# Kernel optimization log

Measured on AMD Instinct MI355X. Metric: run time of the kernel, lower is better.

## Reference

```python
import jax, jax.numpy as jnp
import numpy as np

B, N, L = 1, 2048, 256
H, E = 24, 128
D = H * E          # query_dim = inner_dim = 3072
P = 1536           # added_kv_proj_dim
EPS = 1e-5


def _rope_tables(n, e):
    pos = np.arange(n, dtype=np.float32)
    inv_freq = 1.0 / (10000.0 ** (np.arange(0, e, 2, dtype=np.float32) / e))
    ang = pos[:, None] * inv_freq[None, :]          # [n, e/2]
    ang = np.repeat(ang, 2, axis=-1)                # interleaved pairs -> [n, e]
    return np.cos(ang).astype(np.float32), np.sin(ang).astype(np.float32)


def _trans_mat(e):
    # rotate-pairs matrix: (x @ tm)[2i] = -x[2i+1], (x @ tm)[2i+1] = x[2i]
    tm = np.zeros((e, e), dtype=np.float32)
    idx = np.arange(0, e, 2)
    tm[idx + 1, idx] = -1.0
    tm[idx, idx + 1] = 1.0
    return tm


def setup_inputs() -> dict:
    key = jax.random.key(0)
    ks = jax.random.split(key, 16)
    s = 0.02
    cos, sin = _rope_tables(N, E)
    return {
        "spatial": jax.random.normal(ks[0], (B, N, D), jnp.float32),
        "prompt": jax.random.normal(ks[1], (B, L, P), jnp.float32),
        "w_qkv": jax.random.normal(ks[2], (D, 3 * D), jnp.float32) * s,
        "w_add_qkv": jax.random.normal(ks[3], (P, 3 * D), jnp.float32) * s,
        "b_add_qkv": jax.random.normal(ks[4], (3 * D,), jnp.float32) * s,
        "norm_q_w": jnp.ones((E,), jnp.float32),
        "norm_k_w": jnp.ones((E,), jnp.float32),
        "norm_add_q_w": jnp.ones((E,), jnp.float32),
        "norm_add_k_w": jnp.ones((E,), jnp.float32),
        "w_out": jax.random.normal(ks[5], (D, D), jnp.float32) * s,
        "b_out": jax.random.normal(ks[6], (D,), jnp.float32) * s,
        "w_add_out": jax.random.normal(ks[7], (D, D), jnp.float32) * s,
        "b_add_out": jax.random.normal(ks[8], (D,), jnp.float32) * s,
        "rope_cos": jnp.asarray(cos),
        "rope_sin": jnp.asarray(sin),
        "trans_mat": jnp.asarray(_trans_mat(E)),
        "N": N,
    }


def _rms(x, w):
    return x * jax.lax.rsqrt(jnp.mean(x * x, axis=-1, keepdims=True) + EPS) * w


def _split_heads(x, h, e):
    b, s, _ = x.shape
    return x.reshape(b, s, h, e).transpose(0, 2, 1, 3)  # [B,H,S,E]


def reference(spatial, prompt, w_qkv, w_add_qkv, b_add_qkv,
              norm_q_w, norm_k_w, norm_add_q_w, norm_add_k_w,
              w_out, b_out, w_add_out, b_add_out,
              rope_cos, rope_sin, trans_mat, N):
    e = norm_q_w.shape[0]
    h = w_qkv.shape[1] // (3 * e)
    b, n, _ = spatial.shape

    # fused QKV for spatial stream (no bias)
    q, k, v = jnp.split(spatial @ w_qkv, 3, axis=-1)
    q, k, v = (_split_heads(t, h, e) for t in (q, k, v))   # [B,H,N,E]
    q = _rms(q, norm_q_w)
    k = _rms(k, norm_k_w)

    # fused QKV for prompt stream (with bias)
    aq, ak, av = jnp.split(prompt @ w_add_qkv + b_add_qkv, 3, axis=-1)
    aq, ak, av = (_split_heads(t, h, e) for t in (aq, ak, av))  # [B,H,L,E]
    aq = _rms(aq, norm_add_q_w)
    ak = _rms(ak, norm_add_k_w)

    # RoPE on spatial q/k: x*cos + (x@trans_mat)*sin
    def rope(x):
        return x * rope_cos + jnp.einsum('bhne,ef->bhnf', x, trans_mat) * rope_sin
    q = rope(q)
    k = rope(k)

    # joint attention, 'rear' strategy: prompt KV appended after spatial KV
    qf = jnp.concatenate([q, aq], axis=2)   # [B,H,N+L,E]
    kf = jnp.concatenate([k, ak], axis=2)
    vf = jnp.concatenate([v, av], axis=2)
    scale = 1.0 / jnp.sqrt(jnp.float32(e))
    scores = jnp.einsum('bhqe,bhke->bhqk', qf, kf) * scale
    attn = jax.nn.softmax(scores, axis=-1)
    out = jnp.einsum('bhqk,bhke->bhqe', attn, vf)           # [B,H,N+L,E]

    def merge(x):
        return x.transpose(0, 2, 1, 3).reshape(b, x.shape[2], h * e)

    spatial_out = merge(out[:, :, :n]) @ w_out + b_out      # [B,N,D]
    prompt_out = merge(out[:, :, n:]) @ w_add_out + b_add_out  # [B,L,D]
    return spatial_out, prompt_out
```

## Files before the change

kernel.cpp:

```cpp
#include <hip/hip_runtime.h>
#include <cstdint>
#include <cstddef>

typedef __attribute__((ext_vector_type(8))) short short8;
typedef __attribute__((ext_vector_type(4))) float f32x4;
typedef __attribute__((ext_vector_type(16))) float f32x16;

#define DEVI static __device__ __forceinline__

DEVI float bf2f(unsigned short b) {
  union { unsigned int u; float f; } v; v.u = ((unsigned int)b) << 16; return v.f;
}
DEVI unsigned short f2bf(float f) {
  union { float f; unsigned int u; } v; v.f = f;
  unsigned int r = v.u + 0x7fffu + ((v.u >> 16) & 1u);
  return (unsigned short)(r >> 16);
}
DEVI unsigned int pk2(float a, float b) {
  union { float f; unsigned int u; } ua, ub; ua.f = a; ub.f = b;
  return ((ua.u + 0x8000u) >> 16) | ((ub.u + 0x8000u) & 0xffff0000u);
}

DEVI void gload16(const void* g, void* l) {
  __builtin_amdgcn_global_load_lds(
      (const __attribute__((address_space(1))) void*)g,
      (__attribute__((address_space(3))) void*)l, 16, 0, 0);
}

DEVI void drain_ldsdma() {
  asm volatile("s_waitcnt vmcnt(0)" ::: "memory");
  __builtin_amdgcn_sched_barrier(0);
}

DEVI void tr_body(const float* in, unsigned short* out, int Kd, int Nd,
                  int n0, int k0, unsigned short (*tile)[72], int t)
{
  int r = t >> 2, cg = (t & 3) * 16;
  const float* src = in + (size_t)(k0 + r) * Nd + n0 + cg;
#pragma unroll
  for (int q = 0; q < 16; q += 4) {
    float4 f = *(const float4*)(src + q);
    ushort4 u;
    u.x = f2bf(f.x); u.y = f2bf(f.y); u.z = f2bf(f.z); u.w = f2bf(f.w);
    *(ushort4*)&tile[r][cg + q] = u;
  }
  __syncthreads();
  unsigned int p[8];
#pragma unroll
  for (int q = 0; q < 8; ++q)
    p[q] = (unsigned int)tile[cg + 2*q][r] | ((unsigned int)tile[cg + 2*q + 1][r] << 16);
  unsigned short* dst = out + (size_t)(n0 + r) * Kd + k0 + cg;
  *(uint4*)dst       = make_uint4(p[0], p[1], p[2], p[3]);
  *(uint4*)(dst + 8) = make_uint4(p[4], p[5], p[6], p[7]);
}

__global__ __launch_bounds__(256) void prep(
    const float* __restrict__ spatial, unsigned short* __restrict__ spat_bf,
    const float* __restrict__ prompt,  unsigned short* __restrict__ prom_bf,
    const float* __restrict__ w_qkv,   const float* __restrict__ w_add_qkv,
    unsigned short* __restrict__ wTq,  unsigned short* __restrict__ wTaq)
{
  __shared__ unsigned short tile[64][72];
  const int b = blockIdx.x;
  if (b < 2048) {
    const int n4a = 2048 * 3072 / 4, n4b = 256 * 1536 / 4;
    int i = b * 256 + threadIdx.x;
    int stride = 2048 * 256;
    int total = n4a + n4b;
    for (; i < total; i += stride) {
      const float4* src = (i < n4a) ? &((const float4*)spatial)[i]
                                    : &((const float4*)prompt)[i - n4a];
      ushort4* dst = (i < n4a) ? &((ushort4*)spat_bf)[i] : &((ushort4*)prom_bf)[i - n4a];
      float4 f = *src;
      ushort4 u;
      u.x = f2bf(f.x); u.y = f2bf(f.y); u.z = f2bf(f.z); u.w = f2bf(f.w);
      *dst = u;
    }
  } else {
    int bb = b - 2048;
    int bx = bb % 144, y = bb / 144;
    const float* in;  unsigned short* out;  int Kd, k0;
    if (y < 48) { in = w_qkv;     out = wTq;  Kd = 3072; k0 = y * 64; }
    else        { in = w_add_qkv; out = wTaq; Kd = 1536; k0 = (y - 48) * 64; }
    tr_body(in, out, Kd, 9216, bx * 64, k0, tile, threadIdx.x);
  }
}

__global__ __launch_bounds__(256) void transpose_wout(
    const float* __restrict__ w_out, const float* __restrict__ w_add_out,
    unsigned short* __restrict__ wTo, unsigned short* __restrict__ wTao)
{
  __shared__ unsigned short tile[64][72];
  const float* in = blockIdx.z ? w_add_out : w_out;
  unsigned short* out = blockIdx.z ? wTao : wTo;
  tr_body(in, out, 3072, 3072, blockIdx.x * 64, blockIdx.y * 64, tile, threadIdx.x);
}

__global__ __launch_bounds__(256) void transpose_bf16_64(
    const unsigned short* __restrict__ in, unsigned short* __restrict__ out,
    int rows, int cols)
{
  __shared__ unsigned short tile[64][72];
  size_t hoff = (size_t)blockIdx.z * rows * cols;
  int e0 = blockIdx.x * 64, s0 = blockIdx.y * 64;
  int t = threadIdx.x;
  int r = t >> 2, cg = (t & 3) * 16;
  const unsigned short* src = in + hoff + (size_t)(s0 + r) * cols + e0 + cg;
  *(uint4*)&tile[r][cg]     = *(const uint4*)src;
  *(uint4*)&tile[r][cg + 8] = *(const uint4*)(src + 8);
  __syncthreads();
  unsigned int p[8];
#pragma unroll
  for (int q = 0; q < 8; ++q)
    p[q] = (unsigned int)tile[cg + 2*q][r] | ((unsigned int)tile[cg + 2*q + 1][r] << 16);
  unsigned short* dst = out + hoff + (size_t)(e0 + r) * rows + s0 + cg;
  *(uint4*)dst       = make_uint4(p[0], p[1], p[2], p[3]);
  *(uint4*)(dst + 8) = make_uint4(p[4], p[5], p[6], p[7]);
}

__global__ __launch_bounds__(256, 4) void gemm_qkv2(
    const unsigned short* __restrict__ Aspat, const unsigned short* __restrict__ Aprom,
    const unsigned short* __restrict__ Btq, const unsigned short* __restrict__ Btaq,
    const float* __restrict__ biasp, unsigned short* __restrict__ Cout)
{
  __shared__ unsigned short lsA[128 * 64];
  __shared__ unsigned short lsB[128 * 64];
  const int tid = threadIdx.x;
  const int w = tid >> 6, lane = tid & 63;
  const int wr = w >> 1, wc = w & 1;
  const int l15 = lane & 15, lhi = lane >> 4;
  const int wg = blockIdx.x;
  const int swz = (wg & 7) * 162 + (wg >> 3);
  const int bx = swz / 18, by = swz - bx * 18;
  const bool pr = by >= 16;
  const int K = pr ? 1536 : 3072;

  f32x4 acc[4][4];
#pragma unroll
  for (int i = 0; i < 4; ++i)
#pragma unroll
    for (int j = 0; j < 4; ++j) acc[i][j] = (f32x4){0.f, 0.f, 0.f, 0.f};

  int srcoff[4];
#pragma unroll
  for (int j = 0; j < 4; ++j) {
    int c = j * 256 + tid;
    int row = c >> 3;
    int sl = (c & 7) ^ (row & 7);
    srcoff[j] = row * K + sl * 8;
  }
  const int wb = w * 1024;
  const unsigned short* Abase = pr ? (Aprom + (size_t)((by - 16) * 128) * 1536)
                                   : (Aspat + (size_t)(by * 128) * 3072);
  const unsigned short* Bbase = (pr ? Btaq : Btq) + (size_t)(bx * 128) * K;

  for (int k0 = 0; k0 < K; k0 += 64) {
#pragma unroll
    for (int j = 0; j < 4; ++j) {
      gload16(Abase + srcoff[j] + k0, (char*)lsA + j * 4096 + wb);
      gload16(Bbase + srcoff[j] + k0, (char*)lsB + j * 4096 + wb);
    }
    __syncthreads();
#pragma unroll
    for (int kk = 0; kk < 2; ++kk) {
      const int sl = ((kk << 2) + lhi) ^ (l15 & 7);
      short8 af[4], bf[4];
#pragma unroll
      for (int t = 0; t < 4; ++t) {
        af[t] = *(const short8*)((char*)lsA + (wr * 64 + t * 16 + l15) * 128 + (sl << 4));
        bf[t] = *(const short8*)((char*)lsB + (wc * 64 + t * 16 + l15) * 128 + (sl << 4));
      }
#pragma unroll
      for (int mt = 0; mt < 4; ++mt)
#pragma unroll
        for (int nt = 0; nt < 4; ++nt)
          acc[mt][nt] = __builtin_amdgcn_mfma_f32_16x16x32_bf16(af[mt], bf[nt], acc[mt][nt], 0, 0, 0);
    }
    __syncthreads();
  }

  const int nbase = bx * 128 + wc * 64;
  const int mbase = by * 128 + wr * 64;
  float bv[4] = {0.f, 0.f, 0.f, 0.f};
  if (pr) {
#pragma unroll
    for (int nt = 0; nt < 4; ++nt) bv[nt] = biasp[nbase + nt * 16 + l15];
  }
#pragma unroll
  for (int mt = 0; mt < 4; ++mt)
#pragma unroll
    for (int nt = 0; nt < 4; ++nt) {
#pragma unroll
      for (int r2 = 0; r2 < 4; ++r2) {
        int m = mbase + mt * 16 + lhi * 4 + r2;
        int n = nbase + nt * 16 + l15;
        Cout[(size_t)m * 9216 + n] = f2bf(acc[mt][nt][r2] + bv[nt]);
      }
    }
}

__global__ __launch_bounds__(256, 4) void gemm_out2(
    const unsigned short* __restrict__ A,
    const unsigned short* __restrict__ Bt0, const float* __restrict__ b0,
    const unsigned short* __restrict__ Bt1, const float* __restrict__ b1,
    float* __restrict__ C)
{
  __shared__ unsigned short lsA[128 * 64];
  __shared__ unsigned short lsB[128 * 64];
  const int tid = threadIdx.x;
  const int w = tid >> 6, lane = tid & 63;
  const int wr = w >> 1, wc = w & 1;
  const int l15 = lane & 15, lhi = lane >> 4;
  const int wg = blockIdx.x;
  const int swz = (wg & 7) * 54 + (wg >> 3);
  const int bx = swz / 18, by = swz - bx * 18;
  const bool pr = by >= 16;

  f32x4 acc[4][4];
#pragma unroll
  for (int i = 0; i < 4; ++i)
#pragma unroll
    for (int j = 0; j < 4; ++j) acc[i][j] = (f32x4){0.f, 0.f, 0.f, 0.f};

  int srcoff[4];
#pragma unroll
  for (int j = 0; j < 4; ++j) {
    int c = j * 256 + tid;
    int row = c >> 3;
    int sl = (c & 7) ^ (row & 7);
    srcoff[j] = row * 3072 + sl * 8;
  }
  const int wb = w * 1024;
  const unsigned short* Abase = A + (size_t)(by * 128) * 3072;
  const unsigned short* Bbase = (pr ? Bt1 : Bt0) + (size_t)(bx * 128) * 3072;
  const float* bias = pr ? b1 : b0;

  for (int k0 = 0; k0 < 3072; k0 += 64) {
#pragma unroll
    for (int j = 0; j < 4; ++j) {
      gload16(Abase + srcoff[j] + k0, (char*)lsA + j * 4096 + wb);
      gload16(Bbase + srcoff[j] + k0, (char*)lsB + j * 4096 + wb);
    }
    __syncthreads();
#pragma unroll
    for (int kk = 0; kk < 2; ++kk) {
      const int sl = ((kk << 2) + lhi) ^ (l15 & 7);
      short8 af[4], bf[4];
#pragma unroll
      for (int t = 0; t < 4; ++t) {
        af[t] = *(const short8*)((char*)lsA + (wr * 64 + t * 16 + l15) * 128 + (sl << 4));
        bf[t] = *(const short8*)((char*)lsB + (wc * 64 + t * 16 + l15) * 128 + (sl << 4));
      }
#pragma unroll
      for (int mt = 0; mt < 4; ++mt)
#pragma unroll
        for (int nt = 0; nt < 4; ++nt)
          acc[mt][nt] = __builtin_amdgcn_mfma_f32_16x16x32_bf16(af[mt], bf[nt], acc[mt][nt], 0, 0, 0);
    }
    __syncthreads();
  }

  const int nbase = bx * 128 + wc * 64;
  const int mbase = by * 128 + wr * 64;
  float bv[4];
#pragma unroll
  for (int nt = 0; nt < 4; ++nt) bv[nt] = bias[nbase + nt * 16 + l15];
#pragma unroll
  for (int mt = 0; mt < 4; ++mt)
#pragma unroll
    for (int nt = 0; nt < 4; ++nt) {
#pragma unroll
      for (int r2 = 0; r2 < 4; ++r2) {
        int m = mbase + mt * 16 + lhi * 4 + r2;
        int n = nbase + nt * 16 + l15;
        C[(size_t)m * 3072 + n] = acc[mt][nt][r2] + bv[nt];
      }
    }
}

__global__ __launch_bounds__(256) void fuse_rms_rope(
    const unsigned short* __restrict__ qkv,
    const unsigned short* __restrict__ aqkv,
    const float* __restrict__ nq, const float* __restrict__ nk,
    const float* __restrict__ naq, const float* __restrict__ nak,
    const float* __restrict__ ctab, const float* __restrict__ stab,
    unsigned short* __restrict__ Qf, unsigned short* __restrict__ Kf,
    unsigned short* __restrict__ Vf)
{
  int wid = blockIdx.x * 4 + (threadIdx.x >> 6);
  int lane = threadIdx.x & 63;
  int h = wid / 2304, s = wid % 2304;
  bool sp = (s < 2048);
  const unsigned short* src = sp ? (qkv + (size_t)s * 9216)
                                 : (aqkv + (size_t)(s - 2048) * 9216);
  int e = lane * 2;
  ushort2 qu = *(const ushort2*)&src[h * 128 + e];
  ushort2 ku = *(const ushort2*)&src[3072 + h * 128 + e];
  ushort2 vu = *(const ushort2*)&src[6144 + h * 128 + e];
  float q0 = bf2f(qu.x), q1 = bf2f(qu.y);
  float k0 = bf2f(ku.x), k1 = bf2f(ku.y);
  float sq = q0 * q0 + q1 * q1, sk = k0 * k0 + k1 * k1;
#pragma unroll
  for (int mm = 1; mm < 64; mm <<= 1) {
    sq += __shfl_xor(sq, mm);
    sk += __shfl_xor(sk, mm);
  }
  float rq = rsqrtf(sq * (1.f / 128.f) + 1e-5f);
  float rk = rsqrtf(sk * (1.f / 128.f) + 1e-5f);
  const float* wq = sp ? nq : naq;
  const float* wk = sp ? nk : nak;
  q0 *= rq * wq[e]; q1 *= rq * wq[e + 1];
  k0 *= rk * wk[e]; k1 *= rk * wk[e + 1];
  if (sp) {
    float c0 = ctab[s * 128 + e], c1 = ctab[s * 128 + e + 1];
    float s0 = stab[s * 128 + e], s1 = stab[s * 128 + e + 1];
    float a0 = q0 * c0 - q1 * s0, a1 = q1 * c1 + q0 * s1;
    float b0 = k0 * c0 - k1 * s0, b1 = k1 * c1 + k0 * s1;
    q0 = a0; q1 = a1; k0 = b0; k1 = b1;
  }
  const float scale = 0.08838834764831845f * 1.4426950408889634f;
  q0 *= scale; q1 *= scale;
  size_t o = (size_t)h * 2304 * 128 + (size_t)s * 128 + e;
  *(ushort2*)&Qf[o] = make_ushort2(f2bf(q0), f2bf(q1));
  *(ushort2*)&Kf[o] = make_ushort2(f2bf(k0), f2bf(k1));
  *(ushort2*)&Vf[o] = vu;
}

__global__ __launch_bounds__(256, 2) void attn_fwd(
    const unsigned short* __restrict__ Qf, const unsigned short* __restrict__ Kf,
    const unsigned short* __restrict__ Vt, unsigned short* __restrict__ Om)
{
  __shared__ unsigned short lsK[2][64 * 128];
  __shared__ unsigned short lsV[2][128 * 64];
  int wg = blockIdx.x;
  int swz = (wg & 7) * 54 + (wg >> 3);
  int h = swz / 18, qt = swz - h * 18;
  int q0 = qt * 128;
  int tid = threadIdx.x, w = tid >> 6, lane = tid & 63;
  int l31 = lane & 31, hh = lane >> 5;
  const size_t headO = (size_t)h * 2304 * 128;

  short8 qf[8];
  {
    const unsigned short* qrow = Qf + headO + (size_t)(q0 + w * 32 + l31) * 128 + hh * 8;
#pragma unroll
    for (int s = 0; s < 8; ++s)
      qf[s] = *(const short8*)(qrow + s * 16);
  }

  float m_run = 0.0f, lsum = 0.f;
  f32x16 accO[4];
#pragma unroll
  for (int dt = 0; dt < 4; ++dt)
#pragma unroll
    for (int i = 0; i < 16; ++i) accO[dt][i] = 0.f;

  size_t kGo[4], vGo[4];
  int loff[4];
#pragma unroll
  for (int j = 0; j < 4; ++j) {
    int c = j * 256 + w * 64 + lane;
    int krow = c >> 4, kcol = (c & 15) ^ (krow & 15);
    int sr = c >> 4, lg = (c & 15) ^ (sr & 15);
    int vrow = sr * 2 + (lg >> 3), vcol = lg & 7;
    kGo[j] = (size_t)krow * 128 + kcol * 8;
    vGo[j] = (size_t)vrow * 2304 + vcol * 8;
    loff[j] = (j * 256 + w * 64) * 16;
  }
  const unsigned short* kbase0 = Kf + headO;
  const unsigned short* vbase0 = Vt + headO;

  auto stage = [&](int kb2, int b) {
    const unsigned short* kb_ = kbase0 + (size_t)kb2 * 128;
    const unsigned short* vb_ = vbase0 + kb2;
#pragma unroll
    for (int j = 0; j < 4; ++j) {
      gload16(kb_ + kGo[j], (char*)lsK[b] + loff[j]);
      gload16(vb_ + vGo[j], (char*)lsV[b] + loff[j]);
    }
  };

  stage(0, 0);
  int cur = 0;

  for (int kb = 0; kb < 2304; kb += 64) {
    drain_ldsdma();
    __syncthreads();
    if (kb + 64 < 2304) stage(kb + 64, cur ^ 1);

    f32x16 accS[2];
#pragma unroll
    for (int t = 0; t < 2; ++t)
#pragma unroll
      for (int i = 0; i < 16; ++i) accS[t][i] = 0.f;
    __builtin_amdgcn_s_setprio(1);
#pragma unroll
    for (int t = 0; t < 2; ++t) {
      const int row = l31 + t * 32;
      const int rsw = row & 15;
#pragma unroll
      for (int s = 0; s < 8; ++s) {
        short8 kfr = *(const short8*)((char*)lsK[cur] + row * 256 +
                        (((s * 2 + hh) ^ rsw) << 4));
        accS[t] = __builtin_amdgcn_mfma_f32_32x32x16_bf16(kfr, qf[s], accS[t], 0, 0, 0);
      }
    }

#pragma unroll
    for (int ks = 0; ks < 4; ++ks) {
      const int t = ks >> 1;
      const int qlo = 8 * (ks & 1);
      float p0 = __builtin_amdgcn_exp2f(accS[t][qlo + 0] - m_run);
      float p1 = __builtin_amdgcn_exp2f(accS[t][qlo + 1] - m_run);
      float p2 = __builtin_amdgcn_exp2f(accS[t][qlo + 2] - m_run);
      float p3 = __builtin_amdgcn_exp2f(accS[t][qlo + 3] - m_run);
      float p4 = __builtin_amdgcn_exp2f(accS[t][qlo + 4] - m_run);
      float p5 = __builtin_amdgcn_exp2f(accS[t][qlo + 5] - m_run);
      float p6 = __builtin_amdgcn_exp2f(accS[t][qlo + 6] - m_run);
      float p7 = __builtin_amdgcn_exp2f(accS[t][qlo + 7] - m_run);
      lsum += ((p0 + p1) + (p2 + p3)) + ((p4 + p5) + (p6 + p7));
      unsigned int wlo0 = pk2(p0, p1);
      unsigned int wlo1 = pk2(p2, p3);
      unsigned int whi0 = pk2(p4, p5);
      unsigned int whi1 = pk2(p6, p7);
      unsigned int r0 = __shfl_xor(hh ? wlo0 : whi0, 32);
      unsigned int r1 = __shfl_xor(hh ? wlo1 : whi1, 32);
      unsigned int fw0 = hh ? r0 : wlo0;
      unsigned int fw1 = hh ? r1 : wlo1;
      unsigned int fw2 = hh ? whi0 : r0;
      unsigned int fw3 = hh ? whi1 : r1;
      unsigned int fwa[4] = {fw0, fw1, fw2, fw3};
      short8 paf = *(short8*)fwa;
#pragma unroll
      for (int dt = 0; dt < 4; ++dt) {
        const int row = dt * 32 + l31;
        const int sr = row >> 1;
        const int g = (((row & 1) << 3) | (ks * 2 + hh)) ^ (sr & 15);
        short8 vfr = *(const short8*)((char*)lsV[cur] + sr * 256 + (g << 4));
        accO[dt] = __builtin_amdgcn_mfma_f32_32x32x16_bf16(paf, vfr, accO[dt], 0, 0, 0);
      }
    }
    __builtin_amdgcn_s_setprio(0);

    float lm = accS[0][0];
#pragma unroll
    for (int t = 0; t < 2; ++t)
#pragma unroll
      for (int i = 0; i < 16; ++i) lm = fmaxf(lm, accS[t][i]);
    float lmx = fmaxf(lm, __shfl_xor(lm, 32));
    if (!__all(lmx <= m_run + 11.0f)) {
      float mnew = fmaxf(m_run, lmx);
      float corr = __builtin_amdgcn_exp2f(m_run - mnew);
      lsum *= corr;
      float corrq[16];
#pragma unroll
      for (int r = 0; r < 16; ++r)
        corrq[r] = __shfl(corr, ((r & 3) + 8 * (r >> 2) + 4 * hh) | (lane & 32));
#pragma unroll
      for (int dt = 0; dt < 4; ++dt)
#pragma unroll
        for (int r = 0; r < 16; ++r) accO[dt][r] *= corrq[r];
      m_run = mnew;
    }
    cur ^= 1;
  }

  lsum += __shfl_xor(lsum, 32);
  float inv = 1.0f / lsum;
  float invq[16];
#pragma unroll
  for (int r = 0; r < 16; ++r)
    invq[r] = __shfl(inv, ((r & 3) + 8 * (r >> 2) + 4 * hh) | (lane & 32));
#pragma unroll
  for (int dt = 0; dt < 4; ++dt)
#pragma unroll
    for (int r = 0; r < 16; ++r) {
      int qrow = (r & 3) + 8 * (r >> 2) + 4 * hh;
      int row = q0 + w * 32 + qrow;
      Om[(size_t)row * 3072 + h * 128 + dt * 32 + l31] = f2bf(accO[dt][r] * invq[r]);
    }
}

extern "C" void kernel_launch(void* const* d_in, const int* in_sizes, int n_in,
                              void* d_out, int out_size, void* d_ws, size_t ws_size,
                              hipStream_t stream)
{
  const float* spatial      = (const float*)d_in[0];
  const float* prompt       = (const float*)d_in[1];
  const float* w_qkv        = (const float*)d_in[2];
  const float* w_add_qkv    = (const float*)d_in[3];
  const float* b_add_qkv    = (const float*)d_in[4];
  const float* norm_q_w     = (const float*)d_in[5];
  const float* norm_k_w     = (const float*)d_in[6];
  const float* norm_add_q_w = (const float*)d_in[7];
  const float* norm_add_k_w = (const float*)d_in[8];
  const float* w_out        = (const float*)d_in[9];
  const float* b_out        = (const float*)d_in[10];
  const float* w_add_out    = (const float*)d_in[11];
  const float* b_add_out    = (const float*)d_in[12];
  const float* rope_cos     = (const float*)d_in[13];
  const float* rope_sin     = (const float*)d_in[14];

  constexpr size_t O_WTQ  = 0;
  constexpr size_t O_WTAQ = 56623104;
  constexpr size_t O_SPAT = 84934656;
  constexpr size_t O_PROM = 97517568;
  constexpr size_t O_QKV  = 98304000;
  constexpr size_t O_AQKV = 136052736;
  constexpr size_t O_QF   = 140771328;
  constexpr size_t O_KF   = 154927104;
  constexpr size_t O_VF   = 169082880;
  constexpr size_t TOTAL  = 183238656;
  constexpr size_t O_WTO  = O_WTQ;
  constexpr size_t O_WTAO = O_WTQ + 18874368;
  constexpr size_t O_VT   = O_QKV;
  constexpr size_t O_ATTN = O_WTAQ;
  if (ws_size < TOTAL) return;

  char* ws = (char*)d_ws;
  unsigned short* wTq      = (unsigned short*)(ws + O_WTQ);
  unsigned short* wTaq     = (unsigned short*)(ws + O_WTAQ);
  unsigned short* spat_bf  = (unsigned short*)(ws + O_SPAT);
  unsigned short* prom_bf  = (unsigned short*)(ws + O_PROM);
  unsigned short* qkv_s    = (unsigned short*)(ws + O_QKV);
  unsigned short* aqkv     = (unsigned short*)(ws + O_AQKV);
  unsigned short* Qf       = (unsigned short*)(ws + O_QF);
  unsigned short* Kf       = (unsigned short*)(ws + O_KF);
  unsigned short* Vf       = (unsigned short*)(ws + O_VF);
  unsigned short* wTo      = (unsigned short*)(ws + O_WTO);
  unsigned short* wTao     = (unsigned short*)(ws + O_WTAO);
  unsigned short* Vt       = (unsigned short*)(ws + O_VT);
  unsigned short* attn_out = (unsigned short*)(ws + O_ATTN);

  prep<<<12416, 256, 0, stream>>>(spatial, spat_bf, prompt, prom_bf,
                                  w_qkv, w_add_qkv, wTq, wTaq);
  gemm_qkv2<<<1296, 256, 0, stream>>>(spat_bf, prom_bf, wTq, wTaq, b_add_qkv, qkv_s);
  fuse_rms_rope<<<13824, 256, 0, stream>>>(qkv_s, aqkv, norm_q_w, norm_k_w,
                                           norm_add_q_w, norm_add_k_w,
                                           rope_cos, rope_sin, Qf, Kf, Vf);
  transpose_bf16_64<<<dim3(2, 36, 24), 256, 0, stream>>>(Vf, Vt, 2304, 128);
  attn_fwd<<<432, 256, 0, stream>>>(Qf, Kf, Vt, attn_out);
  transpose_wout<<<dim3(48, 48, 2), 256, 0, stream>>>(w_out, w_add_out, wTo, wTao);
  gemm_out2<<<432, 256, 0, stream>>>(attn_out, wTo, b_out, wTao, b_add_out,
                                     (float*)d_out);
}
```

Before: 389.1 us.

## Split attention KV range in two with log-sum-exp combine kernel

The attention kernel now splits each head's key/value sequence into two halves, launching 864 workgroups instead of 432 so that more of the GPU's compute units are busy. Each half writes a bf16 partial output plus a per-row log-sum-exp. A new combine kernel merges the two halves with softmax weights. The V LDS buffer is single-buffered and staged after a second barrier so occupancy can rise to 3 waves per SIMD, and the row max is now computed inside the exp loop. The cost is an extra kernel launch, extra global traffic for the partials, an additional bf16 rounding step, and a V load that is no longer overlapped with compute.

```diff
diff --git a/kernel.cpp b/kernel.cpp
--- a/kernel.cpp
+++ b/kernel.cpp
@@ -326,16 +326,22 @@
   *(ushort2*)&Vf[o] = vu;
 }
 
-__global__ __launch_bounds__(256, 2) void attn_fwd(
+__global__ __launch_bounds__(256, 3) void attn_part(
     const unsigned short* __restrict__ Qf, const unsigned short* __restrict__ Kf,
-    const unsigned short* __restrict__ Vt, unsigned short* __restrict__ Om)
+    const unsigned short* __restrict__ Vt,
+    unsigned short* __restrict__ part1, unsigned short* __restrict__ part2,
+    float* __restrict__ Ls1, float* __restrict__ Ls2)
 {
   __shared__ unsigned short lsK[2][64 * 128];
-  __shared__ unsigned short lsV[2][128 * 64];
+  __shared__ unsigned short lsV[128 * 64];
   int wg = blockIdx.x;
-  int swz = (wg & 7) * 54 + (wg >> 3);
-  int h = swz / 18, qt = swz - h * 18;
+  int idx = (wg & 7) * 108 + (wg >> 3);
+  int h = idx / 36, rem = idx - h * 36;
+  int qt = rem >> 1, kvh = rem & 1;
   int q0 = qt * 128;
+  const int kb0 = kvh * 1152;
+  unsigned short* pOut = kvh ? part2 : part1;
+  float* Ls = kvh ? Ls2 : Ls1;
   int tid = threadIdx.x, w = tid >> 6, lane = tid & 63;
   int l31 = lane & 31, hh = lane >> 5;
   const size_t headO = (size_t)h * 2304 * 128;
@@ -370,23 +376,28 @@
   const unsigned short* kbase0 = Kf + headO;
   const unsigned short* vbase0 = Vt + headO;
 
-  auto stage = [&](int kb2, int b) {
+  auto stageK = [&](int kb2, int b) {
     const unsigned short* kb_ = kbase0 + (size_t)kb2 * 128;
+#pragma unroll
+    for (int j = 0; j < 4; ++j)
+      gload16(kb_ + kGo[j], (char*)lsK[b] + loff[j]);
+  };
+  auto stageV = [&](int kb2) {
     const unsigned short* vb_ = vbase0 + kb2;
 #pragma unroll
-    for (int j = 0; j < 4; ++j) {
-      gload16(kb_ + kGo[j], (char*)lsK[b] + loff[j]);
-      gload16(vb_ + vGo[j], (char*)lsV[b] + loff[j]);
-    }
+    for (int j = 0; j < 4; ++j)
+      gload16(vb_ + vGo[j], (char*)lsV + loff[j]);
   };
 
-  stage(0, 0);
+  stageK(kb0, 0);
+  stageV(kb0);
   int cur = 0;
 
-  for (int kb = 0; kb < 2304; kb += 64) {
+  for (int it = 0; it < 18; ++it) {
+    const int kb = kb0 + it * 64;
     drain_ldsdma();
     __syncthreads();
-    if (kb + 64 < 2304) stage(kb + 64, cur ^ 1);
+    if (it + 1 < 18) stageK(kb + 64, cur ^ 1);
 
     f32x16 accS[2];
 #pragma unroll
@@ -406,18 +417,25 @@
       }
     }
 
+    float lm = -1e30f;
 #pragma unroll
     for (int ks = 0; ks < 4; ++ks) {
       const int t = ks >> 1;
       const int qlo = 8 * (ks & 1);
-      float p0 = __builtin_amdgcn_exp2f(accS[t][qlo + 0] - m_run);
-      float p1 = __builtin_amdgcn_exp2f(accS[t][qlo + 1] - m_run);
-      float p2 = __builtin_amdgcn_exp2f(accS[t][qlo + 2] - m_run);
-      float p3 = __builtin_amdgcn_exp2f(accS[t][qlo + 3] - m_run);
-      float p4 = __builtin_amdgcn_exp2f(accS[t][qlo + 4] - m_run);
-      float p5 = __builtin_amdgcn_exp2f(accS[t][qlo + 5] - m_run);
-      float p6 = __builtin_amdgcn_exp2f(accS[t][qlo + 6] - m_run);
-      float p7 = __builtin_amdgcn_exp2f(accS[t][qlo + 7] - m_run);
+      float s0 = accS[t][qlo + 0], s1 = accS[t][qlo + 1];
+      float s2 = accS[t][qlo + 2], s3 = accS[t][qlo + 3];
+      float s4 = accS[t][qlo + 4], s5 = accS[t][qlo + 5];
+      float s6 = accS[t][qlo + 6], s7 = accS[t][qlo + 7];
+      lm = fmaxf(lm, fmaxf(fmaxf(fmaxf(s0, s1), fmaxf(s2, s3)),
+                           fmaxf(fmaxf(s4, s5), fmaxf(s6, s7))));
+      float p0 = __builtin_amdgcn_exp2f(s0 - m_run);
+      float p1 = __builtin_amdgcn_exp2f(s1 - m_run);
+      float p2 = __builtin_amdgcn_exp2f(s2 - m_run);
+      float p3 = __builtin_amdgcn_exp2f(s3 - m_run);
+      float p4 = __builtin_amdgcn_exp2f(s4 - m_run);
+      float p5 = __builtin_amdgcn_exp2f(s5 - m_run);
+      float p6 = __builtin_amdgcn_exp2f(s6 - m_run);
+      float p7 = __builtin_amdgcn_exp2f(s7 - m_run);
       lsum += ((p0 + p1) + (p2 + p3)) + ((p4 + p5) + (p6 + p7));
       unsigned int wlo0 = pk2(p0, p1);
       unsigned int wlo1 = pk2(p2, p3);
@@ -436,17 +454,12 @@
         const int row = dt * 32 + l31;
         const int sr = row >> 1;
         const int g = (((row & 1) << 3) | (ks * 2 + hh)) ^ (sr & 15);
-        short8 vfr = *(const short8*)((char*)lsV[cur] + sr * 256 + (g << 4));
+        short8 vfr = *(const short8*)((char*)lsV + sr * 256 + (g << 4));
         accO[dt] = __builtin_amdgcn_mfma_f32_32x32x16_bf16(paf, vfr, accO[dt], 0, 0, 0);
       }
     }
     __builtin_amdgcn_s_setprio(0);
 
-    float lm = accS[0][0];
-#pragma unroll
-    for (int t = 0; t < 2; ++t)
-#pragma unroll
-      for (int i = 0; i < 16; ++i) lm = fmaxf(lm, accS[t][i]);
     float lmx = fmaxf(lm, __shfl_xor(lm, 32));
     if (!__all(lmx <= m_run + 11.0f)) {
       float mnew = fmaxf(m_run, lmx);
@@ -462,11 +475,16 @@
         for (int r = 0; r < 16; ++r) accO[dt][r] *= corrq[r];
       m_run = mnew;
     }
+
+    __syncthreads();
+    if (it + 1 < 18) stageV(kb + 64);
     cur ^= 1;
   }
 
   lsum += __shfl_xor(lsum, 32);
   float inv = 1.0f / lsum;
+  if (hh == 0)
+    Ls[h * 2304 + q0 + w * 32 + l31] = m_run + __log2f(lsum);
   float invq[16];
 #pragma unroll
   for (int r = 0; r < 16; ++r)
@@ -477,8 +495,31 @@
     for (int r = 0; r < 16; ++r) {
       int qrow = (r & 3) + 8 * (r >> 2) + 4 * hh;
       int row = q0 + w * 32 + qrow;
-      Om[(size_t)row * 3072 + h * 128 + dt * 32 + l31] = f2bf(accO[dt][r] * invq[r]);
-    }
+      pOut[(size_t)row * 3072 + h * 128 + dt * 32 + l31] = f2bf(accO[dt][r] * invq[r]);
+    }
+}
+
+__global__ __launch_bounds__(256) void attn_combine(
+    const unsigned short* __restrict__ p1, const unsigned short* __restrict__ p2,
+    const float* __restrict__ Ls1, const float* __restrict__ Ls2,
+    unsigned short* __restrict__ out)
+{
+  int wid = blockIdx.x * 4 + (threadIdx.x >> 6);
+  int lane = threadIdx.x & 63;
+  int h = wid / 2304, row = wid - h * 2304;
+  float l1 = Ls1[h * 2304 + row], l2 = Ls2[h * 2304 + row];
+  float mx = fmaxf(l1, l2);
+  float wa = __builtin_amdgcn_exp2f(l1 - mx);
+  float wb = __builtin_amdgcn_exp2f(l2 - mx);
+  float inv = 1.0f / (wa + wb);
+  wa *= inv; wb *= inv;
+  size_t o = (size_t)row * 3072 + h * 128 + lane * 2;
+  ushort2 a = *(const ushort2*)&p1[o];
+  ushort2 b = *(const ushort2*)&p2[o];
+  ushort2 r;
+  r.x = f2bf(wa * bf2f(a.x) + wb * bf2f(b.x));
+  r.y = f2bf(wa * bf2f(a.y) + wb * bf2f(b.y));
+  *(ushort2*)&out[o] = r;
 }
 
 extern "C" void kernel_launch(void* const* d_in, const int* in_sizes, int n_in,
@@ -511,10 +552,14 @@
   constexpr size_t O_KF   = 154927104;
   constexpr size_t O_VF   = 169082880;
   constexpr size_t TOTAL  = 183238656;
-  constexpr size_t O_WTO  = O_WTQ;
-  constexpr size_t O_WTAO = O_WTQ + 18874368;
-  constexpr size_t O_VT   = O_QKV;
-  constexpr size_t O_ATTN = O_WTAQ;
+  constexpr size_t O_VT   = 0;
+  constexpr size_t O_WTO  = 0;
+  constexpr size_t O_WTAO = 18874368;
+  constexpr size_t O_P1   = 37748736;
+  constexpr size_t O_AO   = 66060288;
+  constexpr size_t O_P2   = 94371840;
+  constexpr size_t O_LS1  = 122683392;
+  constexpr size_t O_LS2  = 122904576;
   if (ws_size < TOTAL) return;
 
   char* ws = (char*)d_ws;
@@ -527,10 +572,14 @@
   unsigned short* Qf       = (unsigned short*)(ws + O_QF);
   unsigned short* Kf       = (unsigned short*)(ws + O_KF);
   unsigned short* Vf       = (unsigned short*)(ws + O_VF);
+  unsigned short* Vt       = (unsigned short*)(ws + O_VT);
   unsigned short* wTo      = (unsigned short*)(ws + O_WTO);
   unsigned short* wTao     = (unsigned short*)(ws + O_WTAO);
-  unsigned short* Vt       = (unsigned short*)(ws + O_VT);
-  unsigned short* attn_out = (unsigned short*)(ws + O_ATTN);
+  unsigned short* part1    = (unsigned short*)(ws + O_P1);
+  unsigned short* part2    = (unsigned short*)(ws + O_P2);
+  unsigned short* attn_out = (unsigned short*)(ws + O_AO);
+  float* Ls1 = (float*)(ws + O_LS1);
+  float* Ls2 = (float*)(ws + O_LS2);
 
   prep<<<12416, 256, 0, stream>>>(spatial, spat_bf, prompt, prom_bf,
                                   w_qkv, w_add_qkv, wTq, wTaq);
@@ -539,7 +588,8 @@
                                            norm_add_q_w, norm_add_k_w,
                                            rope_cos, rope_sin, Qf, Kf, Vf);
   transpose_bf16_64<<<dim3(2, 36, 24), 256, 0, stream>>>(Vf, Vt, 2304, 128);
-  attn_fwd<<<432, 256, 0, stream>>>(Qf, Kf, Vt, attn_out);
+  attn_part<<<864, 256, 0, stream>>>(Qf, Kf, Vt, part1, part2, Ls1, Ls2);
+  attn_combine<<<13824, 256, 0, stream>>>(part1, part2, Ls1, Ls2, attn_out);
   transpose_wout<<<dim3(48, 48, 2), 256, 0, stream>>>(w_out, w_add_out, wTo, wTao);
   gemm_out2<<<432, 256, 0, stream>>>(attn_out, wTo, b_out, wTao, b_add_out,
                                      (float*)d_out);
```

Result: slower. 481.3 us (+23.7%).
